# Kernel optimization log

Hardware: AMD Instinct MI355X
Metric: run time of the kernel (lower is better)

Reference implementation:

```python
import jax, jax.numpy as jnp
import numpy as np


def setup_inputs() -> dict:
    key = jax.random.key(0)
    k1, k2, k3, k4 = jax.random.split(key, 4)
    E, d, N = 800000, 64, 50000
    M = jax.random.normal(k1, (E, d), dtype=jnp.float32)
    a = jax.random.normal(k2, (d,), dtype=jnp.float32)
    edge_index = jax.random.randint(k3, (2, E), 0, N, dtype=jnp.int64)
    rev_index = jax.random.randint(k4, (E,), 0, E, dtype=jnp.int64)
    return {"M": M, "a": a, "edge_index": edge_index, "rev_index": rev_index, "dim_size": N}


def reference(M, a, edge_index, rev_index, dim_size):
    src, dest = edge_index[0], edge_index[1]
    # attention scores per message, segment-softmax over destination node
    score = M @ a  # [E]
    smax = jax.ops.segment_max(score, dest, num_segments=dim_size)  # [N]
    ex = jnp.exp(score - smax[dest])  # [E]
    denom = jax.ops.segment_sum(ex, dest, num_segments=dim_size)  # [N]
    alpha = (ex / denom[dest])[:, None]  # [E, 1]
    aM = alpha * M  # [E, d]
    M_v = jax.ops.segment_sum(aM, dest, num_segments=dim_size)  # [N, d]
    # directed=True: subtract reverse message contribution
    return M_v[src] - aM[rev_index]
```

## Files before the change

### kernel.cpp

```cpp
#include <hip/hip_runtime.h>
#include <float.h>


#define THREADS 256

typedef float f32x4 __attribute__((ext_vector_type(4)));

__global__ void k_zero(int4* __restrict__ p, int n4) {
    int i = blockIdx.x * blockDim.x + threadIdx.x;
    if (i < n4) p[i] = make_int4(0, 0, 0, 0);
}

__global__ void k_hist(const int* __restrict__ dest,
                       int* __restrict__ counts, int E) {
    int e = blockIdx.x * blockDim.x + threadIdx.x;
    if (e >= E) return;
    atomicAdd(&counts[dest[e]], 1);
}

__global__ void k_alloc(const int* __restrict__ counts,
                        int* __restrict__ total,
                        int* __restrict__ offsets,
                        int* __restrict__ cursor,
                        int N) {
    int n    = blockIdx.x * blockDim.x + threadIdx.x;
    int lane = threadIdx.x & 63;
    int c = (n < N) ? counts[n] : 0;
    int x = c;
    #pragma unroll
    for (int off = 1; off < 64; off <<= 1) {
        int y = __shfl_up(x, off, 64);
        if (lane >= off) x += y;
    }
    int wsum = __shfl(x, 63, 64);
    int base = 0;
    if (lane == 63) base = atomicAdd(total, wsum);
    base = __shfl(base, 63, 64);
    if (n < N) {
        int my = base + x - c;
        offsets[n] = my;
        cursor[n]  = my;
    }
}

__global__ void k_score_fill(const float4* __restrict__ M4,
                             const float4* __restrict__ a4,
                             const int* __restrict__ dest,
                             int* __restrict__ cursor,
                             int* __restrict__ sorted_eid,
                             float* __restrict__ sorted_score,
                             int E) {
    long long gid = (long long)blockIdx.x * blockDim.x + threadIdx.x;
    int e  = (int)(gid >> 4);
    int sl = (int)(gid & 15);
    if (e >= E) return;
    float4 m  = M4[(size_t)e * 16 + sl];
    float4 av = a4[sl];
    float v = m.x * av.x + m.y * av.y + m.z * av.z + m.w * av.w;
    v += __shfl_xor(v, 1, 64);
    v += __shfl_xor(v, 2, 64);
    v += __shfl_xor(v, 4, 64);
    v += __shfl_xor(v, 8, 64);
    if (sl == 0) {
        int pos = atomicAdd(&cursor[dest[e]], 1);
        sorted_eid[pos]   = e;
        sorted_score[pos] = v;
    }
}

__global__ void k_aggregate(const float4* __restrict__ M4,
                            const float* __restrict__ sorted_score,
                            const int* __restrict__ sorted_eid,
                            const int* __restrict__ offsets,
                            const int* __restrict__ counts,
                            float4* __restrict__ Mv4,
                            float* __restrict__ alpha,
                            int N) {
    long long gid = (long long)blockIdx.x * blockDim.x + threadIdx.x;
    int n    = (int)(gid >> 6);
    int lane = (int)(gid & 63);
    if (n >= N) return;
    int beg = offsets[n];
    int deg = counts[n];
    int end = beg + deg;
    int grp = lane >> 4;
    int sl  = lane & 15;

    float4 acc = make_float4(0.f, 0.f, 0.f, 0.f);

    if (deg <= 64) {
        int   eid = 0;
        float sc  = -FLT_MAX;
        if (lane < deg) {
            eid = sorted_eid[beg + lane];
            sc  = sorted_score[beg + lane];
        }
        float m = sc;
        #pragma unroll
        for (int off = 32; off; off >>= 1)
            m = fmaxf(m, __shfl_xor(m, off, 64));
        float exr = (lane < deg) ? expf(sc - m) : 0.f;
        float ds  = exr;
        #pragma unroll
        for (int off = 32; off; off >>= 1)
            ds += __shfl_xor(ds, off, 64);
        float inv = ds > 0.f ? 1.0f / ds : 0.0f;
        if (lane < deg) alpha[eid] = exr * inv;
        int iters = (deg + 3) >> 2;
        for (int k = 0; k < iters; ++k) {
            int i = grp + 4 * k;
            float ex = __shfl(exr, i, 64);
            int   e  = __shfl(eid, i, 64);
            if (i < deg) {
                float4 mm = M4[(size_t)e * 16 + sl];
                acc.x += ex * mm.x;
                acc.y += ex * mm.y;
                acc.z += ex * mm.z;
                acc.w += ex * mm.w;
            }
        }
        acc.x += __shfl_xor(acc.x, 16, 64);  acc.x += __shfl_xor(acc.x, 32, 64);
        acc.y += __shfl_xor(acc.y, 16, 64);  acc.y += __shfl_xor(acc.y, 32, 64);
        acc.z += __shfl_xor(acc.z, 16, 64);  acc.z += __shfl_xor(acc.z, 32, 64);
        acc.w += __shfl_xor(acc.w, 16, 64);  acc.w += __shfl_xor(acc.w, 32, 64);
        if (lane < 16) {
            float4 o;
            o.x = acc.x * inv; o.y = acc.y * inv;
            o.z = acc.z * inv; o.w = acc.w * inv;
            Mv4[(size_t)n * 16 + lane] = o;
        }
    } else {
        float m = -FLT_MAX;
        for (int i = beg + lane; i < end; i += 64)
            m = fmaxf(m, sorted_score[i]);
        #pragma unroll
        for (int off = 32; off; off >>= 1)
            m = fmaxf(m, __shfl_xor(m, off, 64));
        float dsum = 0.f;
        for (int i = beg + grp; i < end; i += 4) {
            int e = sorted_eid[i];
            float ex = expf(sorted_score[i] - m);
            if (sl == 0) dsum += ex;
            float4 mm = M4[(size_t)e * 16 + sl];
            acc.x += ex * mm.x;
            acc.y += ex * mm.y;
            acc.z += ex * mm.z;
            acc.w += ex * mm.w;
        }
        dsum += __shfl_xor(dsum, 16, 64);
        dsum += __shfl_xor(dsum, 32, 64);
        float dtot = __shfl(dsum, 0, 64);
        float inv = dtot > 0.f ? 1.0f / dtot : 0.0f;
        for (int i = beg + lane; i < end; i += 64) {
            alpha[sorted_eid[i]] = expf(sorted_score[i] - m) * inv;
        }
        acc.x += __shfl_xor(acc.x, 16, 64);  acc.x += __shfl_xor(acc.x, 32, 64);
        acc.y += __shfl_xor(acc.y, 16, 64);  acc.y += __shfl_xor(acc.y, 32, 64);
        acc.z += __shfl_xor(acc.z, 16, 64);  acc.z += __shfl_xor(acc.z, 32, 64);
        acc.w += __shfl_xor(acc.w, 16, 64);  acc.w += __shfl_xor(acc.w, 32, 64);
        if (lane < 16) {
            float4 o;
            o.x = acc.x * inv; o.y = acc.y * inv;
            o.z = acc.z * inv; o.w = acc.w * inv;
            Mv4[(size_t)n * 16 + lane] = o;
        }
    }
}

__global__ void k_out(const float4* __restrict__ M4,
                      const float4* __restrict__ Mv4,
                      const float* __restrict__ alpha,
                      const int* __restrict__ src,
                      const int* __restrict__ rev,
                      f32x4* __restrict__ out4,
                      int E) {
    long long gid = (long long)blockIdx.x * blockDim.x + threadIdx.x;
    int e  = (int)(gid >> 4);
    int sl = (int)(gid & 15);
    if (e >= E) return;
    int s    = src[e];
    int r    = rev[e];
    float al = alpha[r];
    float4 mv = Mv4[(size_t)s * 16 + sl];
    float4 mr = M4[(size_t)r * 16 + sl];
    f32x4 o;
    o.x = mv.x - al * mr.x;
    o.y = mv.y - al * mr.y;
    o.z = mv.z - al * mr.z;
    o.w = mv.w - al * mr.w;
    __builtin_nontemporal_store(o, &out4[(size_t)e * 16 + sl]);
}

extern "C" void kernel_launch(void* const* d_in, const int* in_sizes, int n_in,
                              void* d_out, int out_size, void* d_ws, size_t ws_size,
                              hipStream_t stream) {
    const float* M  = (const float*)d_in[0];
    const float* a  = (const float*)d_in[1];
    const int* eidx = (const int*)d_in[2];
    const int* rev  = (const int*)d_in[3];
    const int N = 50000;
    const int E = in_sizes[3];

    const int* src  = eidx;
    const int* dest = eidx + E;

    char* ws = (char*)d_ws;
    float* Mv          = (float*)ws; ws += (size_t)N * 64 * 4;
    float* sorted_score= (float*)ws; ws += (size_t)E * 4;
    float* alpha       = (float*)ws; ws += (size_t)E * 4;
    int*   sorted_eid  = (int*)ws;   ws += (size_t)E * 4;
    int*   counts      = (int*)ws;   ws += (size_t)(N + 4) * 4;
    int*   offsets     = (int*)ws;   ws += (size_t)N * 4;
    int*   cursor      = (int*)ws;   ws += (size_t)N * 4;
    int*   total       = counts + N;

    long long tE16 = (long long)E * 16;
    int blocksE16 = (int)((tE16 + THREADS - 1) / THREADS);
    int blocksE   = (E + THREADS - 1) / THREADS;
    int blocksN   = (N + THREADS - 1) / THREADS;
    int blocksN64 = (int)(((long long)N * 64 + THREADS - 1) / THREADS);
    int n4        = (N + 4) / 4;
    int blocksZ   = (n4 + THREADS - 1) / THREADS;

    k_zero<<<blocksZ, THREADS, 0, stream>>>((int4*)counts, n4);
    k_hist<<<blocksE, THREADS, 0, stream>>>(dest, counts, E);
    k_alloc<<<blocksN, THREADS, 0, stream>>>(counts, total, offsets, cursor, N);
    k_score_fill<<<blocksE16, THREADS, 0, stream>>>(
        (const float4*)M, (const float4*)a, dest, cursor,
        sorted_eid, sorted_score, E);
    k_aggregate<<<blocksN64, THREADS, 0, stream>>>(
        (const float4*)M, sorted_score, sorted_eid, offsets, counts,
        (float4*)Mv, alpha, N);
    k_out<<<blocksE16, THREADS, 0, stream>>>(
        (const float4*)M, (const float4*)Mv, alpha, src, rev,
        (f32x4*)d_out, E);
}
```

Baseline: 259.2 us.

## Fuse all stages into one cooperative persistent kernel with grid syncs

Replaces the six separate kernel launches with a single cooperative persistent kernel. It runs zero, histogram, scan, score-fill, aggregate and output as grid-stride phases separated by grid.sync(). The aim is to remove per-launch overhead and the gaps between kernels. The cost is grid-wide barriers and occupancy limited to what fits co-resident, with the old multi-kernel path kept as a fallback.

```diff
diff --git a/kernel.cpp b/kernel.cpp
--- a/kernel.cpp
+++ b/kernel.cpp
@@ -1,59 +1,20 @@
 #include <hip/hip_runtime.h>
+#include <hip/hip_cooperative_groups.h>
 #include <float.h>
 
+namespace cg = cooperative_groups;
+
 
 #define THREADS 256
 
 typedef float f32x4 __attribute__((ext_vector_type(4)));
 
-__global__ void k_zero(int4* __restrict__ p, int n4) {
-    int i = blockIdx.x * blockDim.x + threadIdx.x;
-    if (i < n4) p[i] = make_int4(0, 0, 0, 0);
-}
-
-__global__ void k_hist(const int* __restrict__ dest,
-                       int* __restrict__ counts, int E) {
-    int e = blockIdx.x * blockDim.x + threadIdx.x;
-    if (e >= E) return;
-    atomicAdd(&counts[dest[e]], 1);
-}
-
-__global__ void k_alloc(const int* __restrict__ counts,
-                        int* __restrict__ total,
-                        int* __restrict__ offsets,
-                        int* __restrict__ cursor,
-                        int N) {
-    int n    = blockIdx.x * blockDim.x + threadIdx.x;
-    int lane = threadIdx.x & 63;
-    int c = (n < N) ? counts[n] : 0;
-    int x = c;
-    #pragma unroll
-    for (int off = 1; off < 64; off <<= 1) {
-        int y = __shfl_up(x, off, 64);
-        if (lane >= off) x += y;
-    }
-    int wsum = __shfl(x, 63, 64);
-    int base = 0;
-    if (lane == 63) base = atomicAdd(total, wsum);
-    base = __shfl(base, 63, 64);
-    if (n < N) {
-        int my = base + x - c;
-        offsets[n] = my;
-        cursor[n]  = my;
-    }
-}
-
-__global__ void k_score_fill(const float4* __restrict__ M4,
-                             const float4* __restrict__ a4,
-                             const int* __restrict__ dest,
-                             int* __restrict__ cursor,
-                             int* __restrict__ sorted_eid,
-                             float* __restrict__ sorted_score,
-                             int E) {
-    long long gid = (long long)blockIdx.x * blockDim.x + threadIdx.x;
-    int e  = (int)(gid >> 4);
-    int sl = (int)(gid & 15);
-    if (e >= E) return;
+
+__device__ __forceinline__ void score_fill_edge(
+    const float4* __restrict__ M4, const float4* __restrict__ a4,
+    const int* __restrict__ dest, int* __restrict__ cursor,
+    int* __restrict__ sorted_eid, float* __restrict__ sorted_score,
+    int e, int sl) {
     float4 m  = M4[(size_t)e * 16 + sl];
     float4 av = a4[sl];
     float v = m.x * av.x + m.y * av.y + m.z * av.z + m.w * av.w;
@@ -68,24 +29,16 @@
     }
 }
 
-__global__ void k_aggregate(const float4* __restrict__ M4,
-                            const float* __restrict__ sorted_score,
-                            const int* __restrict__ sorted_eid,
-                            const int* __restrict__ offsets,
-                            const int* __restrict__ counts,
-                            float4* __restrict__ Mv4,
-                            float* __restrict__ alpha,
-                            int N) {
-    long long gid = (long long)blockIdx.x * blockDim.x + threadIdx.x;
-    int n    = (int)(gid >> 6);
-    int lane = (int)(gid & 63);
-    if (n >= N) return;
+__device__ __forceinline__ void agg_node(
+    const float4* __restrict__ M4, const float* __restrict__ sorted_score,
+    const int* __restrict__ sorted_eid, const int* __restrict__ offsets,
+    const int* __restrict__ counts, float4* __restrict__ Mv4,
+    float* __restrict__ alpha, int n, int lane) {
     int beg = offsets[n];
     int deg = counts[n];
     int end = beg + deg;
     int grp = lane >> 4;
     int sl  = lane & 15;
-
     float4 acc = make_float4(0.f, 0.f, 0.f, 0.f);
 
     if (deg <= 64) {
@@ -151,9 +104,8 @@
         dsum += __shfl_xor(dsum, 32, 64);
         float dtot = __shfl(dsum, 0, 64);
         float inv = dtot > 0.f ? 1.0f / dtot : 0.0f;
-        for (int i = beg + lane; i < end; i += 64) {
+        for (int i = beg + lane; i < end; i += 64)
             alpha[sorted_eid[i]] = expf(sorted_score[i] - m) * inv;
-        }
         acc.x += __shfl_xor(acc.x, 16, 64);  acc.x += __shfl_xor(acc.x, 32, 64);
         acc.y += __shfl_xor(acc.y, 16, 64);  acc.y += __shfl_xor(acc.y, 32, 64);
         acc.z += __shfl_xor(acc.z, 16, 64);  acc.z += __shfl_xor(acc.z, 32, 64);
@@ -167,17 +119,11 @@
     }
 }
 
-__global__ void k_out(const float4* __restrict__ M4,
-                      const float4* __restrict__ Mv4,
-                      const float* __restrict__ alpha,
-                      const int* __restrict__ src,
-                      const int* __restrict__ rev,
-                      f32x4* __restrict__ out4,
-                      int E) {
-    long long gid = (long long)blockIdx.x * blockDim.x + threadIdx.x;
-    int e  = (int)(gid >> 4);
-    int sl = (int)(gid & 15);
-    if (e >= E) return;
+__device__ __forceinline__ void out_edge(
+    const float4* __restrict__ M4, const float4* __restrict__ Mv4,
+    const float* __restrict__ alpha, const int* __restrict__ src,
+    const int* __restrict__ rev, f32x4* __restrict__ out4,
+    int e, int sl) {
     int s    = src[e];
     int r    = rev[e];
     float al = alpha[r];
@@ -191,6 +137,151 @@
     __builtin_nontemporal_store(o, &out4[(size_t)e * 16 + sl]);
 }
 
+struct Params {
+    const float4* M4; const float4* a4;
+    const int* src; const int* dest; const int* rev;
+    int* counts; int* total; int* offsets; int* cursor;
+    int* sorted_eid; float* sorted_score;
+    float4* Mv4; float* alpha; f32x4* out4;
+    int E; int N;
+};
+
+__global__ __launch_bounds__(THREADS)
+void k_mega(Params p) {
+    cg::grid_group grid = cg::this_grid();
+    const int tid  = blockIdx.x * blockDim.x + threadIdx.x;
+    const int nthr = gridDim.x * blockDim.x;
+    const int lane = threadIdx.x & 63;
+
+    {
+        int n4 = (p.N + 4) >> 2;
+        int4* c4 = (int4*)p.counts;
+        for (int i = tid; i < n4; i += nthr) c4[i] = make_int4(0, 0, 0, 0);
+    }
+    grid.sync();
+
+    for (int e = tid; e < p.E; e += nthr) atomicAdd(&p.counts[p.dest[e]], 1);
+    grid.sync();
+
+    {
+        int wid = tid >> 6;
+        int nw  = nthr >> 6;
+        for (int base = wid * 64; base < p.N; base += nw * 64) {
+            int n = base + lane;
+            int c = (n < p.N) ? p.counts[n] : 0;
+            int x = c;
+            #pragma unroll
+            for (int off = 1; off < 64; off <<= 1) {
+                int y = __shfl_up(x, off, 64);
+                if (lane >= off) x += y;
+            }
+            int wsum = __shfl(x, 63, 64);
+            int b = 0;
+            if (lane == 63) b = atomicAdd(p.total, wsum);
+            b = __shfl(b, 63, 64);
+            if (n < p.N) {
+                int my = b + x - c;
+                p.offsets[n] = my;
+                p.cursor[n]  = my;
+            }
+        }
+    }
+    grid.sync();
+
+    {
+        int g0 = tid >> 4, sl = tid & 15, ng = nthr >> 4;
+        for (int e = g0; e < p.E; e += ng)
+            score_fill_edge(p.M4, p.a4, p.dest, p.cursor,
+                            p.sorted_eid, p.sorted_score, e, sl);
+    }
+    grid.sync();
+
+    {
+        int wid = tid >> 6, nw = nthr >> 6;
+        for (int n = wid; n < p.N; n += nw)
+            agg_node(p.M4, p.sorted_score, p.sorted_eid, p.offsets, p.counts,
+                     p.Mv4, p.alpha, n, lane);
+    }
+    grid.sync();
+
+    {
+        int g0 = tid >> 4, sl = tid & 15, ng = nthr >> 4;
+        for (int e = g0; e < p.E; e += ng)
+            out_edge(p.M4, p.Mv4, p.alpha, p.src, p.rev, p.out4, e, sl);
+    }
+}
+
+__global__ void k_zero(int4* __restrict__ p, int n4) {
+    int i = blockIdx.x * blockDim.x + threadIdx.x;
+    if (i < n4) p[i] = make_int4(0, 0, 0, 0);
+}
+__global__ void k_hist(const int* __restrict__ dest,
+                       int* __restrict__ counts, int E) {
+    int e = blockIdx.x * blockDim.x + threadIdx.x;
+    if (e >= E) return;
+    atomicAdd(&counts[dest[e]], 1);
+}
+__global__ void k_alloc(const int* __restrict__ counts,
+                        int* __restrict__ total,
+                        int* __restrict__ offsets,
+                        int* __restrict__ cursor, int N) {
+    int n    = blockIdx.x * blockDim.x + threadIdx.x;
+    int lane = threadIdx.x & 63;
+    int c = (n < N) ? counts[n] : 0;
+    int x = c;
+    #pragma unroll
+    for (int off = 1; off < 64; off <<= 1) {
+        int y = __shfl_up(x, off, 64);
+        if (lane >= off) x += y;
+    }
+    int wsum = __shfl(x, 63, 64);
+    int b = 0;
+    if (lane == 63) b = atomicAdd(total, wsum);
+    b = __shfl(b, 63, 64);
+    if (n < N) {
+        int my = b + x - c;
+        offsets[n] = my;
+        cursor[n]  = my;
+    }
+}
+__global__ void k_score_fill(const float4* __restrict__ M4,
+                             const float4* __restrict__ a4,
+                             const int* __restrict__ dest,
+                             int* __restrict__ cursor,
+                             int* __restrict__ sorted_eid,
+                             float* __restrict__ sorted_score, int E) {
+    long long gid = (long long)blockIdx.x * blockDim.x + threadIdx.x;
+    int e  = (int)(gid >> 4);
+    int sl = (int)(gid & 15);
+    if (e >= E) return;
+    score_fill_edge(M4, a4, dest, cursor, sorted_eid, sorted_score, e, sl);
+}
+__global__ void k_aggregate(const float4* __restrict__ M4,
+                            const float* __restrict__ sorted_score,
+                            const int* __restrict__ sorted_eid,
+                            const int* __restrict__ offsets,
+                            const int* __restrict__ counts,
+                            float4* __restrict__ Mv4,
+                            float* __restrict__ alpha, int N) {
+    long long gid = (long long)blockIdx.x * blockDim.x + threadIdx.x;
+    int n    = (int)(gid >> 6);
+    int lane = (int)(gid & 63);
+    if (n >= N) return;
+    agg_node(M4, sorted_score, sorted_eid, offsets, counts, Mv4, alpha, n, lane);
+}
+__global__ void k_out(const float4* __restrict__ M4,
+                      const float4* __restrict__ Mv4,
+                      const float* __restrict__ alpha,
+                      const int* __restrict__ src,
+                      const int* __restrict__ rev,
+                      f32x4* __restrict__ out4, int E) {
+    long long gid = (long long)blockIdx.x * blockDim.x + threadIdx.x;
+    int e  = (int)(gid >> 4);
+    int sl = (int)(gid & 15);
+    if (e >= E) return;
+    out_edge(M4, Mv4, alpha, src, rev, out4, e, sl);
+}
+
 extern "C" void kernel_launch(void* const* d_in, const int* in_sizes, int n_in,
                               void* d_out, int out_size, void* d_ws, size_t ws_size,
                               hipStream_t stream) {
@@ -201,18 +292,38 @@
     const int N = 50000;
     const int E = in_sizes[3];
 
-    const int* src  = eidx;
-    const int* dest = eidx + E;
-
     char* ws = (char*)d_ws;
-    float* Mv          = (float*)ws; ws += (size_t)N * 64 * 4;
-    float* sorted_score= (float*)ws; ws += (size_t)E * 4;
-    float* alpha       = (float*)ws; ws += (size_t)E * 4;
-    int*   sorted_eid  = (int*)ws;   ws += (size_t)E * 4;
-    int*   counts      = (int*)ws;   ws += (size_t)(N + 4) * 4;
-    int*   offsets     = (int*)ws;   ws += (size_t)N * 4;
-    int*   cursor      = (int*)ws;   ws += (size_t)N * 4;
-    int*   total       = counts + N;
+    float* Mv           = (float*)ws; ws += (size_t)N * 64 * 4;
+    float* sorted_score = (float*)ws; ws += (size_t)E * 4;
+    float* alpha        = (float*)ws; ws += (size_t)E * 4;
+    int*   sorted_eid   = (int*)ws;   ws += (size_t)E * 4;
+    int*   counts       = (int*)ws;   ws += (size_t)(N + 4) * 4;
+    int*   offsets      = (int*)ws;   ws += (size_t)N * 4;
+    int*   cursor       = (int*)ws;   ws += (size_t)N * 4;
+    int*   total        = counts + N;
+
+    Params p;
+    p.M4 = (const float4*)M;  p.a4 = (const float4*)a;
+    p.src = eidx; p.dest = eidx + E; p.rev = rev;
+    p.counts = counts; p.total = total; p.offsets = offsets; p.cursor = cursor;
+    p.sorted_eid = sorted_eid; p.sorted_score = sorted_score;
+    p.Mv4 = (float4*)Mv; p.alpha = alpha; p.out4 = (f32x4*)d_out;
+    p.E = E; p.N = N;
+
+    int dev = 0;
+    hipGetDevice(&dev);
+    int nCU = 256;
+    hipDeviceGetAttribute(&nCU, hipDeviceAttributeMultiprocessorCount, dev);
+    int occ = 0;
+    hipError_t oe =
+        hipOccupancyMaxActiveBlocksPerMultiprocessor(&occ, k_mega, THREADS, 0);
+    if (oe == hipSuccess && occ >= 1 && nCU >= 1) {
+        int blocks = occ * nCU;
+        void* args[] = { (void*)&p };
+        hipError_t le = hipLaunchCooperativeKernel(
+            (const void*)k_mega, dim3(blocks), dim3(THREADS), args, 0, stream);
+        if (le == hipSuccess) return;
+    }
 
     long long tE16 = (long long)E * 16;
     int blocksE16 = (int)((tE16 + THREADS - 1) / THREADS);
@@ -223,15 +334,13 @@
     int blocksZ   = (n4 + THREADS - 1) / THREADS;
 
     k_zero<<<blocksZ, THREADS, 0, stream>>>((int4*)counts, n4);
-    k_hist<<<blocksE, THREADS, 0, stream>>>(dest, counts, E);
+    k_hist<<<blocksE, THREADS, 0, stream>>>(p.dest, counts, E);
     k_alloc<<<blocksN, THREADS, 0, stream>>>(counts, total, offsets, cursor, N);
     k_score_fill<<<blocksE16, THREADS, 0, stream>>>(
-        (const float4*)M, (const float4*)a, dest, cursor,
-        sorted_eid, sorted_score, E);
+        p.M4, p.a4, p.dest, cursor, sorted_eid, sorted_score, E);
     k_aggregate<<<blocksN64, THREADS, 0, stream>>>(
-        (const float4*)M, sorted_score, sorted_eid, offsets, counts,
+        p.M4, sorted_score, sorted_eid, offsets, counts,
         (float4*)Mv, alpha, N);
     k_out<<<blocksE16, THREADS, 0, stream>>>(
-        (const float4*)M, (const float4*)Mv, alpha, src, rev,
-        (f32x4*)d_out, E);
-}
+        p.M4, (const float4*)Mv, alpha, p.src, p.rev, (f32x4*)d_out, E);
+}
```

After: 938.5 us. 3.62x slower.

## Fuse score computation into aggregation kernel, drop sorted_score buffer

Applied to the files above, without the earlier changes.

The score dot product moves out of the fill kernel and into the per-node aggregate kernel. There it is computed from gathered M rows and staged in shared memory, so the fill kernel becomes a lightweight index scatter and no longer reads all of M. This removes one full streaming pass over M (about 200MB) and the sorted_score buffer. The cost is that the aggregate kernel gathers each M row twice (score, then weighted sum), which may partly hit cache, and it adds a block-wide sync. The high-degree path reuses alpha as temporary score storage.

```diff
diff --git a/kernel.cpp b/kernel.cpp
--- a/kernel.cpp
+++ b/kernel.cpp
@@ -43,58 +43,66 @@
     }
 }
 
-__global__ void k_score_fill(const float4* __restrict__ M4,
-                             const float4* __restrict__ a4,
-                             const int* __restrict__ dest,
-                             int* __restrict__ cursor,
-                             int* __restrict__ sorted_eid,
-                             float* __restrict__ sorted_score,
-                             int E) {
-    long long gid = (long long)blockIdx.x * blockDim.x + threadIdx.x;
-    int e  = (int)(gid >> 4);
-    int sl = (int)(gid & 15);
+__global__ void k_fill(const int* __restrict__ dest,
+                       int* __restrict__ cursor,
+                       int* __restrict__ sorted_eid,
+                       int E) {
+    int e = blockIdx.x * blockDim.x + threadIdx.x;
     if (e >= E) return;
-    float4 m  = M4[(size_t)e * 16 + sl];
-    float4 av = a4[sl];
-    float v = m.x * av.x + m.y * av.y + m.z * av.z + m.w * av.w;
-    v += __shfl_xor(v, 1, 64);
-    v += __shfl_xor(v, 2, 64);
-    v += __shfl_xor(v, 4, 64);
-    v += __shfl_xor(v, 8, 64);
-    if (sl == 0) {
-        int pos = atomicAdd(&cursor[dest[e]], 1);
-        sorted_eid[pos]   = e;
-        sorted_score[pos] = v;
-    }
+    int pos = atomicAdd(&cursor[dest[e]], 1);
+    sorted_eid[pos] = e;
 }
 
 __global__ void k_aggregate(const float4* __restrict__ M4,
-                            const float* __restrict__ sorted_score,
+                            const float4* __restrict__ a4,
                             const int* __restrict__ sorted_eid,
                             const int* __restrict__ offsets,
                             const int* __restrict__ counts,
                             float4* __restrict__ Mv4,
                             float* __restrict__ alpha,
                             int N) {
+    __shared__ float s_sc[THREADS / 64][64];
     long long gid = (long long)blockIdx.x * blockDim.x + threadIdx.x;
-    int n    = (int)(gid >> 6);
-    int lane = (int)(gid & 63);
-    if (n >= N) return;
-    int beg = offsets[n];
-    int deg = counts[n];
-    int end = beg + deg;
-    int grp = lane >> 4;
-    int sl  = lane & 15;
+    int n     = (int)(gid >> 6);
+    int lane  = (int)(gid & 63);
+    int wslot = threadIdx.x >> 6;
+    int grp   = lane >> 4;
+    int sl    = lane & 15;
+
+    bool valid = n < N;
+    int beg = 0, deg = 0;
+    if (valid) { beg = offsets[n]; deg = counts[n]; }
+    bool fast = valid && (deg <= 64);
+
+    float4 avsl = a4[sl];
+    int eid = 0;
+
+    if (fast) {
+        if (lane < deg) eid = sorted_eid[beg + lane];
+        int iters = (deg + 3) >> 2;
+        for (int k = 0; k < iters; ++k) {
+            int i = grp + 4 * k;
+            int e = __shfl(eid, i, 64);
+            float p = 0.f;
+            if (i < deg) {
+                float4 mm = M4[(size_t)e * 16 + sl];
+                p = mm.x * avsl.x + mm.y * avsl.y
+                  + mm.z * avsl.z + mm.w * avsl.w;
+            }
+            p += __shfl_xor(p, 1, 64);
+            p += __shfl_xor(p, 2, 64);
+            p += __shfl_xor(p, 4, 64);
+            p += __shfl_xor(p, 8, 64);
+            if (sl == 0 && i < deg) s_sc[wslot][i] = p;
+        }
+    }
+    __syncthreads();
+    if (!valid) return;
 
     float4 acc = make_float4(0.f, 0.f, 0.f, 0.f);
 
-    if (deg <= 64) {
-        int   eid = 0;
-        float sc  = -FLT_MAX;
-        if (lane < deg) {
-            eid = sorted_eid[beg + lane];
-            sc  = sorted_score[beg + lane];
-        }
+    if (fast) {
+        float sc = (lane < deg) ? s_sc[wslot][lane] : -FLT_MAX;
         float m = sc;
         #pragma unroll
         for (int off = 32; off; off >>= 1)
@@ -130,16 +138,28 @@
             Mv4[(size_t)n * 16 + lane] = o;
         }
     } else {
+        int end = beg + deg;
         float m = -FLT_MAX;
-        for (int i = beg + lane; i < end; i += 64)
-            m = fmaxf(m, sorted_score[i]);
+        for (int i = beg + lane; i < end; i += 64) {
+            int e = sorted_eid[i];
+            const float4* row = M4 + (size_t)e * 16;
+            float s = 0.f;
+            #pragma unroll
+            for (int j = 0; j < 16; ++j) {
+                float4 mm = row[j];
+                float4 av = a4[j];
+                s += mm.x * av.x + mm.y * av.y + mm.z * av.z + mm.w * av.w;
+            }
+            alpha[e] = s;
+            m = fmaxf(m, s);
+        }
         #pragma unroll
         for (int off = 32; off; off >>= 1)
             m = fmaxf(m, __shfl_xor(m, off, 64));
         float dsum = 0.f;
         for (int i = beg + grp; i < end; i += 4) {
             int e = sorted_eid[i];
-            float ex = expf(sorted_score[i] - m);
+            float ex = expf(alpha[e] - m);
             if (sl == 0) dsum += ex;
             float4 mm = M4[(size_t)e * 16 + sl];
             acc.x += ex * mm.x;
@@ -152,7 +172,8 @@
         float dtot = __shfl(dsum, 0, 64);
         float inv = dtot > 0.f ? 1.0f / dtot : 0.0f;
         for (int i = beg + lane; i < end; i += 64) {
-            alpha[sorted_eid[i]] = expf(sorted_score[i] - m) * inv;
+            int e = sorted_eid[i];
+            alpha[e] = expf(alpha[e] - m) * inv;
         }
         acc.x += __shfl_xor(acc.x, 16, 64);  acc.x += __shfl_xor(acc.x, 32, 64);
         acc.y += __shfl_xor(acc.y, 16, 64);  acc.y += __shfl_xor(acc.y, 32, 64);
@@ -205,14 +226,13 @@
     const int* dest = eidx + E;
 
     char* ws = (char*)d_ws;
-    float* Mv          = (float*)ws; ws += (size_t)N * 64 * 4;
-    float* sorted_score= (float*)ws; ws += (size_t)E * 4;
-    float* alpha       = (float*)ws; ws += (size_t)E * 4;
-    int*   sorted_eid  = (int*)ws;   ws += (size_t)E * 4;
-    int*   counts      = (int*)ws;   ws += (size_t)(N + 4) * 4;
-    int*   offsets     = (int*)ws;   ws += (size_t)N * 4;
-    int*   cursor      = (int*)ws;   ws += (size_t)N * 4;
-    int*   total       = counts + N;
+    float* Mv         = (float*)ws; ws += (size_t)N * 64 * 4;
+    float* alpha      = (float*)ws; ws += (size_t)E * 4;
+    int*   sorted_eid = (int*)ws;   ws += (size_t)E * 4;
+    int*   counts     = (int*)ws;   ws += (size_t)(N + 4) * 4;
+    int*   offsets    = (int*)ws;   ws += (size_t)N * 4;
+    int*   cursor     = (int*)ws;   ws += (size_t)N * 4;
+    int*   total      = counts + N;
 
     long long tE16 = (long long)E * 16;
     int blocksE16 = (int)((tE16 + THREADS - 1) / THREADS);
@@ -225,11 +245,9 @@
     k_zero<<<blocksZ, THREADS, 0, stream>>>((int4*)counts, n4);
     k_hist<<<blocksE, THREADS, 0, stream>>>(dest, counts, E);
     k_alloc<<<blocksN, THREADS, 0, stream>>>(counts, total, offsets, cursor, N);
-    k_score_fill<<<blocksE16, THREADS, 0, stream>>>(
-        (const float4*)M, (const float4*)a, dest, cursor,
-        sorted_eid, sorted_score, E);
+    k_fill<<<blocksE, THREADS, 0, stream>>>(dest, cursor, sorted_eid, E);
     k_aggregate<<<blocksN64, THREADS, 0, stream>>>(
-        (const float4*)M, sorted_score, sorted_eid, offsets, counts,
+        (const float4*)M, (const float4*)a, sorted_eid, offsets, counts,
         (float4*)Mv, alpha, N);
     k_out<<<blocksE16, THREADS, 0, stream>>>(
         (const float4*)M, (const float4*)Mv, alpha, src, rev,
```

After: 269.8 us. 4.1% more time.

## Group output rows by reverse index via counting sort to coalesce M reads

Applied to the files above, without the earlier changes.

Adds a counting sort of edges keyed by rev_index (histogram, prefix allocation, fill). The output kernel then iterates over each reverse-target edge q and reads M[q] and alpha[q] contiguously. The aim is to replace the random gather of M[rev] with sequential reads. In exchange, the output writes become scattered by edge id, there are four extra E-sized atomic passes, and per-thread loop counts become uneven because rev multiplicities are irregular.

```diff
diff --git a/kernel.cpp b/kernel.cpp
--- a/kernel.cpp
+++ b/kernel.cpp
@@ -11,21 +11,21 @@
     if (i < n4) p[i] = make_int4(0, 0, 0, 0);
 }
 
-__global__ void k_hist(const int* __restrict__ dest,
+__global__ void k_hist(const int* __restrict__ idx,
                        int* __restrict__ counts, int E) {
     int e = blockIdx.x * blockDim.x + threadIdx.x;
     if (e >= E) return;
-    atomicAdd(&counts[dest[e]], 1);
+    atomicAdd(&counts[idx[e]], 1);
 }
 
 __global__ void k_alloc(const int* __restrict__ counts,
                         int* __restrict__ total,
                         int* __restrict__ offsets,
                         int* __restrict__ cursor,
-                        int N) {
+                        int NB) {
     int n    = blockIdx.x * blockDim.x + threadIdx.x;
     int lane = threadIdx.x & 63;
-    int c = (n < N) ? counts[n] : 0;
+    int c = (n < NB) ? counts[n] : 0;
     int x = c;
     #pragma unroll
     for (int off = 1; off < 64; off <<= 1) {
@@ -36,11 +36,21 @@
     int base = 0;
     if (lane == 63) base = atomicAdd(total, wsum);
     base = __shfl(base, 63, 64);
-    if (n < N) {
+    if (n < NB) {
         int my = base + x - c;
         offsets[n] = my;
         cursor[n]  = my;
     }
+}
+
+__global__ void k_fill(const int* __restrict__ idx,
+                       int* __restrict__ cursor,
+                       int* __restrict__ sorted,
+                       int E) {
+    int e = blockIdx.x * blockDim.x + threadIdx.x;
+    if (e >= E) return;
+    int pos = atomicAdd(&cursor[idx[e]], 1);
+    sorted[pos] = e;
 }
 
 __global__ void k_score_fill(const float4* __restrict__ M4,
@@ -151,9 +161,8 @@
         dsum += __shfl_xor(dsum, 32, 64);
         float dtot = __shfl(dsum, 0, 64);
         float inv = dtot > 0.f ? 1.0f / dtot : 0.0f;
-        for (int i = beg + lane; i < end; i += 64) {
+        for (int i = beg + lane; i < end; i += 64)
             alpha[sorted_eid[i]] = expf(sorted_score[i] - m) * inv;
-        }
         acc.x += __shfl_xor(acc.x, 16, 64);  acc.x += __shfl_xor(acc.x, 32, 64);
         acc.y += __shfl_xor(acc.y, 16, 64);  acc.y += __shfl_xor(acc.y, 32, 64);
         acc.z += __shfl_xor(acc.z, 16, 64);  acc.z += __shfl_xor(acc.z, 32, 64);
@@ -167,28 +176,38 @@
     }
 }
 
-__global__ void k_out(const float4* __restrict__ M4,
-                      const float4* __restrict__ Mv4,
-                      const float* __restrict__ alpha,
-                      const int* __restrict__ src,
-                      const int* __restrict__ rev,
-                      f32x4* __restrict__ out4,
-                      int E) {
+__global__ void k_out_rev(const float4* __restrict__ M4,
+                          const float4* __restrict__ Mv4,
+                          const float* __restrict__ alpha,
+                          const int* __restrict__ src,
+                          const int* __restrict__ counts2,
+                          const int* __restrict__ offsets2,
+                          const int* __restrict__ sorted2,
+                          f32x4* __restrict__ out4,
+                          int E) {
     long long gid = (long long)blockIdx.x * blockDim.x + threadIdx.x;
-    int e  = (int)(gid >> 4);
+    int q  = (int)(gid >> 4);
     int sl = (int)(gid & 15);
-    if (e >= E) return;
-    int s    = src[e];
-    int r    = rev[e];
-    float al = alpha[r];
-    float4 mv = Mv4[(size_t)s * 16 + sl];
-    float4 mr = M4[(size_t)r * 16 + sl];
-    f32x4 o;
-    o.x = mv.x - al * mr.x;
-    o.y = mv.y - al * mr.y;
-    o.z = mv.z - al * mr.z;
-    o.w = mv.w - al * mr.w;
-    __builtin_nontemporal_store(o, &out4[(size_t)e * 16 + sl]);
+    if (q >= E) return;
+    int d2 = counts2[q];
+    if (d2 == 0) return;
+    float  al = alpha[q];
+    float4 mq = M4[(size_t)q * 16 + sl];
+    float4 am;
+    am.x = al * mq.x; am.y = al * mq.y;
+    am.z = al * mq.z; am.w = al * mq.w;
+    int base = offsets2[q];
+    for (int j = 0; j < d2; ++j) {
+        int e = sorted2[base + j];
+        int s = src[e];
+        float4 mv = Mv4[(size_t)s * 16 + sl];
+        f32x4 o;
+        o.x = mv.x - am.x;
+        o.y = mv.y - am.y;
+        o.z = mv.z - am.z;
+        o.w = mv.w - am.w;
+        __builtin_nontemporal_store(o, &out4[(size_t)e * 16 + sl]);
+    }
 }
 
 extern "C" void kernel_launch(void* const* d_in, const int* in_sizes, int n_in,
@@ -205,14 +224,19 @@
     const int* dest = eidx + E;
 
     char* ws = (char*)d_ws;
-    float* Mv          = (float*)ws; ws += (size_t)N * 64 * 4;
-    float* sorted_score= (float*)ws; ws += (size_t)E * 4;
-    float* alpha       = (float*)ws; ws += (size_t)E * 4;
-    int*   sorted_eid  = (int*)ws;   ws += (size_t)E * 4;
-    int*   counts      = (int*)ws;   ws += (size_t)(N + 4) * 4;
-    int*   offsets     = (int*)ws;   ws += (size_t)N * 4;
-    int*   cursor      = (int*)ws;   ws += (size_t)N * 4;
-    int*   total       = counts + N;
+    float* Mv           = (float*)ws; ws += (size_t)N * 64 * 4;
+    float* sorted_score = (float*)ws; ws += (size_t)E * 4;
+    float* alpha        = (float*)ws; ws += (size_t)E * 4;
+    int*   sorted_eid   = (int*)ws;   ws += (size_t)E * 4;
+    int*   counts       = (int*)ws;   ws += (size_t)(N + 4) * 4;
+    int*   offsets      = (int*)ws;   ws += (size_t)N * 4;
+    int*   cursor       = (int*)ws;   ws += (size_t)N * 4;
+    int*   counts2      = (int*)ws;   ws += (size_t)E * 4;
+    int*   offsets2     = (int*)ws;   ws += (size_t)E * 4;
+    int*   cursor2      = (int*)ws;   ws += (size_t)E * 4;
+    int*   sorted2      = (int*)ws;   ws += (size_t)E * 4;
+    int*   total        = counts + N;
+    int*   total2       = counts + N + 1;
 
     long long tE16 = (long long)E * 16;
     int blocksE16 = (int)((tE16 + THREADS - 1) / THREADS);
@@ -221,17 +245,23 @@
     int blocksN64 = (int)(((long long)N * 64 + THREADS - 1) / THREADS);
     int n4        = (N + 4) / 4;
     int blocksZ   = (n4 + THREADS - 1) / THREADS;
+    int e4        = E / 4;
+    int blocksZ2  = (e4 + THREADS - 1) / THREADS;
 
     k_zero<<<blocksZ, THREADS, 0, stream>>>((int4*)counts, n4);
+    k_zero<<<blocksZ2, THREADS, 0, stream>>>((int4*)counts2, e4);
     k_hist<<<blocksE, THREADS, 0, stream>>>(dest, counts, E);
+    k_hist<<<blocksE, THREADS, 0, stream>>>(rev, counts2, E);
     k_alloc<<<blocksN, THREADS, 0, stream>>>(counts, total, offsets, cursor, N);
+    k_alloc<<<blocksE, THREADS, 0, stream>>>(counts2, total2, offsets2, cursor2, E);
     k_score_fill<<<blocksE16, THREADS, 0, stream>>>(
         (const float4*)M, (const float4*)a, dest, cursor,
         sorted_eid, sorted_score, E);
+    k_fill<<<blocksE, THREADS, 0, stream>>>(rev, cursor2, sorted2, E);
     k_aggregate<<<blocksN64, THREADS, 0, stream>>>(
         (const float4*)M, sorted_score, sorted_eid, offsets, counts,
         (float4*)Mv, alpha, N);
-    k_out<<<blocksE16, THREADS, 0, stream>>>(
-        (const float4*)M, (const float4*)Mv, alpha, src, rev,
-        (f32x4*)d_out, E);
-}
+    k_out_rev<<<blocksE16, THREADS, 0, stream>>>(
+        (const float4*)M, (const float4*)Mv, alpha, src,
+        counts2, offsets2, sorted2, (f32x4*)d_out, E);
+}
```

After: 499.2 us. 92.6% more time.
